# Optimization experiments

Hardware: AMD Instinct MI355X
Metric: run time of the kernel (lower is better)

The kernel has to match this reference:

```python
import jax, jax.numpy as jnp
import numpy as np

N_NODES = 50000
N_EDGES = 800000
D_FEAT = 64
N_GRAPHS = 512


def setup_inputs() -> dict:
    key = jax.random.key(0)
    ks = jax.random.split(key, 12)
    edge_index = jax.random.randint(ks[0], (2, N_EDGES), 0, N_NODES, dtype=jnp.int32)
    node_attr = jax.random.normal(ks[1], (N_NODES, D_FEAT), dtype=jnp.float32)
    edge_attr = jax.random.normal(ks[2], (N_EDGES, D_FEAT), dtype=jnp.float32)
    batch = jnp.sort(jax.random.randint(ks[3], (N_NODES,), 0, N_GRAPHS, dtype=jnp.int32))
    s = lambda fan_in: 1.0 / np.sqrt(fan_in)
    W_mpl = jax.random.uniform(ks[4], (3 * D_FEAT, 20), jnp.float32, -s(3 * D_FEAT), s(3 * D_FEAT))
    b_mpl = jnp.zeros((20,), jnp.float32)
    W1 = jax.random.uniform(ks[5], (20, 20), jnp.float32, -s(20), s(20))
    b1 = jnp.zeros((20,), jnp.float32)
    W2 = jax.random.uniform(ks[6], (20, 10), jnp.float32, -s(20), s(20))
    b2 = jnp.zeros((10,), jnp.float32)
    W3 = jax.random.uniform(ks[7], (10, 10), jnp.float32, -s(10), s(10))
    b3 = jnp.zeros((10,), jnp.float32)
    W4 = jax.random.uniform(ks[8], (10, 1), jnp.float32, -s(10), s(10))
    b4 = jnp.zeros((1,), jnp.float32)
    return {"edge_index": edge_index, "node_attr": node_attr, "edge_attr": edge_attr,
            "batch": batch, "W_mpl": W_mpl, "b_mpl": b_mpl, "W1": W1, "b1": b1,
            "W2": W2, "b2": b2, "W3": W3, "b3": b3, "W4": W4, "b4": b4}


def reference(edge_index, node_attr, edge_attr, batch,
              W_mpl, b_mpl, W1, b1, W2, b2, W3, b3, W4, b4):
    src, dst = edge_index[0], edge_index[1]
    # MPL_1: gather -> transform -> scatter-sum to destination nodes. [E, 3D] -> [E, 20]
    msg_in = jnp.concatenate([node_attr[src], node_attr[dst], edge_attr], axis=-1)
    msg = jax.nn.relu(msg_in @ W_mpl + b_mpl)
    x = jax.ops.segment_sum(msg, dst, num_segments=N_NODES)  # [N, 20]
    x = jax.nn.relu(x @ W1 + b1)
    x = jax.nn.relu(x @ W2 + b2)  # [N, 10]
    # segment_coo(reduce='sum') over graph ids -> [G, 10]
    x = jax.ops.segment_sum(x, batch, num_segments=N_GRAPHS)
    x = jax.nn.relu(x @ W3 + b3)
    return x @ W4 + b4  # [G, 1]
```

## Files before the change

kernel.cpp:

```cpp
#include <hip/hip_runtime.h>
#include <hip/hip_fp16.h>

#define DF 64
#define MSG 20
#define HID2 10
#define NODES 50000
#define EDGES 800000
#define GRAPHS 512
#define RSTRIDE 32
#define RS2 12
#define NB1 ((NODES + 255) / 256)
#define WR2 12

#define FMA20(acc, xv, wr) do { \
  float4 w0_ = *(const float4*)((wr) + 0);  float4 w1_ = *(const float4*)((wr) + 4); \
  float4 w2_ = *(const float4*)((wr) + 8);  float4 w3_ = *(const float4*)((wr) + 12); \
  float4 w4_ = *(const float4*)((wr) + 16); \
  acc[0]=fmaf(xv,w0_.x,acc[0]);  acc[1]=fmaf(xv,w0_.y,acc[1]);  acc[2]=fmaf(xv,w0_.z,acc[2]);  acc[3]=fmaf(xv,w0_.w,acc[3]); \
  acc[4]=fmaf(xv,w1_.x,acc[4]);  acc[5]=fmaf(xv,w1_.y,acc[5]);  acc[6]=fmaf(xv,w1_.z,acc[6]);  acc[7]=fmaf(xv,w1_.w,acc[7]); \
  acc[8]=fmaf(xv,w2_.x,acc[8]);  acc[9]=fmaf(xv,w2_.y,acc[9]);  acc[10]=fmaf(xv,w2_.z,acc[10]); acc[11]=fmaf(xv,w2_.w,acc[11]); \
  acc[12]=fmaf(xv,w3_.x,acc[12]); acc[13]=fmaf(xv,w3_.y,acc[13]); acc[14]=fmaf(xv,w3_.z,acc[14]); acc[15]=fmaf(xv,w3_.w,acc[15]); \
  acc[16]=fmaf(xv,w4_.x,acc[16]); acc[17]=fmaf(xv,w4_.y,acc[17]); acc[18]=fmaf(xv,w4_.z,acc[18]); acc[19]=fmaf(xv,w4_.w,acc[19]); \
} while (0)

__global__ __launch_bounds__(256) void zero_cnt_kernel(int* __restrict__ cnt) {
    int i = blockIdx.x * 256 + threadIdx.x;
    int st = gridDim.x * 256;
    for (int k = i; k < NODES; k += st) cnt[k] = 0;
}

__global__ __launch_bounds__(256) void count_kernel(const int* __restrict__ ei, int* __restrict__ cnt) {
    int e = blockIdx.x * 256 + threadIdx.x;
    if (e < EDGES) atomicAdd(&cnt[ei[EDGES + e]], 1);
}

__global__ __launch_bounds__(256) void scan_block(const int* __restrict__ in, int* __restrict__ outx,
                                                  int* __restrict__ bsum, int n) {
    __shared__ int s[256];
    int t = threadIdx.x, i = blockIdx.x * 256 + t;
    int v = (i < n) ? in[i] : 0;
    s[t] = v; __syncthreads();
    for (int off = 1; off < 256; off <<= 1) {
        int x = (t >= off) ? s[t - off] : 0;
        __syncthreads();
        s[t] += x; __syncthreads();
    }
    if (i < n) outx[i] = s[t] - v;
    if (t == 255 && bsum != nullptr) bsum[blockIdx.x] = s[255];
}

__device__ __forceinline__ void store_row_h(__half* dst, const float* acc) {
    union { __half2 h2[16]; uint4 q[4]; } u;
#pragma unroll
    for (int i = 0; i < 10; ++i) u.h2[i] = __floats2half2_rn(acc[2 * i], acc[2 * i + 1]);
#pragma unroll
    for (int i = 10; i < 16; ++i) u.h2[i] = __floats2half2_rn(0.0f, 0.0f);
    uint4* po = (uint4*)dst;
    po[0] = u.q[0]; po[1] = u.q[1]; po[2] = u.q[2]; po[3] = u.q[3];
}

__global__ __launch_bounds__(256) void fixup_pn_kernel(int* __restrict__ rs, int* __restrict__ cur,
                                                       const int* __restrict__ bscan,
                                                       const float* __restrict__ node_attr,
                                                       const float* __restrict__ W,
                                                       __half* __restrict__ Ps, __half* __restrict__ Pd) {
    int i = blockIdx.x * 256 + threadIdx.x;
    if (i < NODES) {
        int r = rs[i] + bscan[blockIdx.x];
        rs[i] = r;
        cur[i] = r;
    }
    if (i == 0) rs[NODES] = EDGES;

    __shared__ float Wss[DF * MSG];
    __shared__ float Wds[DF * MSG];
    for (int k = threadIdx.x; k < DF * MSG; k += 256) {
        Wss[k] = W[k];
        Wds[k] = W[DF * MSG + k];
    }
    __syncthreads();

    int n = i;
    if (n >= NODES) return;

    const float4* nr = (const float4*)(node_attr + (size_t)n * DF);
    float4 x[16];
#pragma unroll
    for (int q = 0; q < 16; ++q) x[q] = nr[q];

    float as[MSG], ad[MSG];
#pragma unroll
    for (int j = 0; j < MSG; ++j) { as[j] = 0.0f; ad[j] = 0.0f; }

#pragma unroll
    for (int k4 = 0; k4 < 16; ++k4) {
        const float* xp = (const float*)&x[k4];
#pragma unroll
        for (int cc = 0; cc < 4; ++cc) {
            int k = k4 * 4 + cc;
            FMA20(as, xp[cc], &Wss[k * MSG]);
            FMA20(ad, xp[cc], &Wds[k * MSG]);
        }
    }

    store_row_h(Ps + (size_t)n * RSTRIDE, as);
    store_row_h(Pd + (size_t)n * RSTRIDE, ad);
}

__global__ __launch_bounds__(256) void gbounds_kernel(const int* __restrict__ batch,
                                                      int* __restrict__ gstart) {
    int i = blockIdx.x * 256 + threadIdx.x;
    if (i < NODES) {
        int b = batch[i];
        int bp = (i == 0) ? -1 : batch[i - 1];
        for (int g = bp + 1; g <= b; ++g) gstart[g] = i;
        if (i == NODES - 1) {
            for (int g = b + 1; g <= GRAPHS; ++g) gstart[g] = NODES;
        }
    }
}

__device__ __forceinline__ __half2 shflx_h2(__half2 v, int mask) {
    int x; __builtin_memcpy(&x, &v, 4);
    x = __shfl_xor(x, mask, 4);
    __half2 r; __builtin_memcpy(&r, &x, 4);
    return r;
}

__device__ __forceinline__ __half2 sel4(int q, __half2 a, __half2 b, __half2 c, __half2 d) {
    __half2 ab = (q & 1) ? b : a;
    __half2 cd = (q & 1) ? d : c;
    return (q & 2) ? cd : ab;
}

__global__ __launch_bounds__(256, 4) void pe_quad_kernel(
    const int* __restrict__ ei,
    const float* __restrict__ edge_attr,
    const float* __restrict__ W, const float* __restrict__ b,
    const __half* __restrict__ Ps,
    int* __restrict__ cur,
    __half* __restrict__ PeP)
{
    __shared__ __half2 Wh2[64 * WR2];
    __shared__ __half2 bh[16];

    const int t = threadIdx.x;
    const int q = t & 3;
    const int e0 = blockIdx.x * 256 + (t >> 2) * 4;

    for (int i = t; i < 64 * WR2; i += 256) {
        int k = i / WR2, j = i - k * WR2;
        __half2 v = __floats2half2_rn(0.0f, 0.0f);
        if (j < 10) v = __floats2half2_rn(W[2 * DF * MSG + k * MSG + 2 * j],
                                          W[2 * DF * MSG + k * MSG + 2 * j + 1]);
        Wh2[i] = v;
    }
    if (t < 16) {
        __half2 v = __floats2half2_rn(0.0f, 0.0f);
        if (t < 10) v = __floats2half2_rn(b[2 * t], b[2 * t + 1]);
        bh[t] = v;
    }

    const int eq = e0 + q;
    const int srcq = ei[eq];
    const int dstq = ei[EDGES + eq];

    const float4* ea4 = (const float4*)edge_attr;
    __half2 xh[4][8];
#pragma unroll
    for (int i = 0; i < 4; ++i) {
        size_t rb = (size_t)(e0 + i) * 16 + q;
        float4 v0 = ea4[rb + 0];
        float4 v1 = ea4[rb + 4];
        float4 v2 = ea4[rb + 8];
        float4 v3 = ea4[rb + 12];
        xh[i][0] = __floats2half2_rn(v0.x, v0.y); xh[i][1] = __floats2half2_rn(v0.z, v0.w);
        xh[i][2] = __floats2half2_rn(v1.x, v1.y); xh[i][3] = __floats2half2_rn(v1.z, v1.w);
        xh[i][4] = __floats2half2_rn(v2.x, v2.y); xh[i][5] = __floats2half2_rn(v2.z, v2.w);
        xh[i][6] = __floats2half2_rn(v3.x, v3.y); xh[i][7] = __floats2half2_rn(v3.z, v3.w);
    }

    __syncthreads();

    __half2 acc[4][10];
#pragma unroll
    for (int i = 0; i < 4; ++i)
#pragma unroll
        for (int j = 0; j < 10; ++j) acc[i][j] = __floats2half2_rn(0.0f, 0.0f);

#pragma unroll
    for (int s = 0; s < 4; ++s) {
#pragma unroll
        for (int d = 0; d < 2; ++d) {
#pragma unroll
            for (int lh = 0; lh < 2; ++lh) {
                int k = s * 16 + q * 4 + 2 * d + lh;
                const __half2* wr = Wh2 + k * WR2;
                __half2 wa[10];
#pragma unroll
                for (int j = 0; j < 10; ++j) wa[j] = wr[j];
#pragma unroll
                for (int i = 0; i < 4; ++i) {
                    __half2 xb = lh ? __high2half2(xh[i][s * 2 + d])
                                    : __low2half2(xh[i][s * 2 + d]);
#pragma unroll
                    for (int j = 0; j < 10; ++j)
                        acc[i][j] = __hfma2(xb, wa[j], acc[i][j]);
                }
            }
        }
    }

#pragma unroll
    for (int i = 0; i < 4; ++i)
#pragma unroll
        for (int j = 0; j < 10; ++j) {
            acc[i][j] = __hadd2(acc[i][j], shflx_h2(acc[i][j], 1));
            acc[i][j] = __hadd2(acc[i][j], shflx_h2(acc[i][j], 2));
        }

#pragma unroll
    for (int i = 0; i < 4; ++i)
#pragma unroll
        for (int j = 0; j < 10; ++j) acc[i][j] = __hadd2(acc[i][j], bh[j]);

    int p = atomicAdd(&cur[dstq], 1);

    const __half2 hz = __floats2half2_rn(0.0f, 0.0f);
#pragma unroll
    for (int i = 0; i < 4; ++i) {
        int pi = __shfl(p, i, 4);
        int si = __shfl(srcq, i, 4);

        __half2 o0 = sel4(q, acc[i][0], acc[i][4], acc[i][8], hz);
        __half2 o1 = sel4(q, acc[i][1], acc[i][5], acc[i][9], hz);
        __half2 o2 = sel4(q, acc[i][2], acc[i][6], hz,        hz);
        __half2 o3 = sel4(q, acc[i][3], acc[i][7], hz,        hz);

        uint4 ps = *(const uint4*)(Ps + (size_t)si * RSTRIDE + q * 8);
        union { uint4 u; __half2 h[4]; } pu; pu.u = ps;
        union { uint4 u; __half2 h[4]; } ou;
        ou.h[0] = __hadd2(o0, pu.h[0]);
        ou.h[1] = __hadd2(o1, pu.h[1]);
        ou.h[2] = __hadd2(o2, pu.h[2]);
        ou.h[3] = __hadd2(o3, pu.h[3]);

        *(uint4*)(PeP + (size_t)pi * RSTRIDE + q * 8) = ou.u;
    }
}

__global__ __launch_bounds__(256, 4) void agg_kernel(const int* __restrict__ rs,
                                                     const __half* __restrict__ PeP,
                                                     const __half* __restrict__ Pd,
                                                     const float* __restrict__ W1, const float* __restrict__ b1,
                                                     const float* __restrict__ W2, const float* __restrict__ b2,
                                                     float* __restrict__ x2) {
    __shared__ float W1s[MSG * MSG], W2s[MSG * HID2], b1s[MSG], b2s[HID2];
    for (int i = threadIdx.x; i < MSG * MSG; i += 256) W1s[i] = W1[i];
    for (int i = threadIdx.x; i < MSG * HID2; i += 256) W2s[i] = W2[i];
    if (threadIdx.x < MSG) b1s[threadIdx.x] = b1[threadIdx.x];
    if (threadIdx.x < HID2) b2s[threadIdx.x] = b2[threadIdx.x];
    __syncthreads();

    int t = threadIdx.x;
    int node = blockIdx.x * 64 + (t >> 2);
    int lane = t & 3;

    float acc[MSG];
#pragma unroll
    for (int j = 0; j < MSG; ++j) acc[j] = 0.0f;

    if (node < NODES) {
        int s0 = rs[node];
        int deg = rs[node + 1] - s0;

        float pd[MSG];
        {
            const uint4* pr = (const uint4*)(Pd + (size_t)node * RSTRIDE);
            union { uint4 q; __half2 h2[4]; } a0, a1;
            union { uint2 q; __half2 h2[2]; } a2;
            a0.q = pr[0]; a1.q = pr[1]; a2.q = *(const uint2*)(pr + 2);
#pragma unroll
            for (int i = 0; i < 4; ++i) {
                float2 f = __half22float2(a0.h2[i]);
                pd[2 * i] = f.x; pd[2 * i + 1] = f.y;
            }
#pragma unroll
            for (int i = 0; i < 4; ++i) {
                float2 f = __half22float2(a1.h2[i]);
                pd[8 + 2 * i] = f.x; pd[9 + 2 * i] = f.y;
            }
#pragma unroll
            for (int i = 0; i < 2; ++i) {
                float2 f = __half22float2(a2.h2[i]);
                pd[16 + 2 * i] = f.x; pd[17 + 2 * i] = f.y;
            }
        }

        for (int i0 = lane; i0 < deg; i0 += 16) {
            uint4 qa[4], qb[4]; uint2 qc[4]; int vm[4];
#pragma unroll
            for (int u = 0; u < 4; ++u) {
                int i = i0 + 4 * u;
                vm[u] = (i < deg);
                if (vm[u]) {
                    const uint4* rp = (const uint4*)(PeP + (size_t)(s0 + i) * RSTRIDE);
                    qa[u] = rp[0]; qb[u] = rp[1]; qc[u] = *(const uint2*)(rp + 2);
                }
            }
#pragma unroll
            for (int u = 0; u < 4; ++u) {
                if (!vm[u]) continue;
                union { uint4 q; __half2 h2[4]; } a0, a1;
                union { uint2 q; __half2 h2[2]; } a2;
                a0.q = qa[u]; a1.q = qb[u]; a2.q = qc[u];
#pragma unroll
                for (int k = 0; k < 4; ++k) {
                    float2 f = __half22float2(a0.h2[k]);
                    acc[2 * k]     += fmaxf(f.x + pd[2 * k], 0.0f);
                    acc[2 * k + 1] += fmaxf(f.y + pd[2 * k + 1], 0.0f);
                }
#pragma unroll
                for (int k = 0; k < 4; ++k) {
                    float2 f = __half22float2(a1.h2[k]);
                    acc[8 + 2 * k] += fmaxf(f.x + pd[8 + 2 * k], 0.0f);
                    acc[9 + 2 * k] += fmaxf(f.y + pd[9 + 2 * k], 0.0f);
                }
#pragma unroll
                for (int k = 0; k < 2; ++k) {
                    float2 f = __half22float2(a2.h2[k]);
                    acc[16 + 2 * k] += fmaxf(f.x + pd[16 + 2 * k], 0.0f);
                    acc[17 + 2 * k] += fmaxf(f.y + pd[17 + 2 * k], 0.0f);
                }
            }
        }
    }

#pragma unroll
    for (int j = 0; j < MSG; ++j) acc[j] += __shfl_xor(acc[j], 1);
#pragma unroll
    for (int j = 0; j < MSG; ++j) acc[j] += __shfl_xor(acc[j], 2);

    if (node < NODES && lane == 0) {
        float t1[MSG];
#pragma unroll
        for (int j = 0; j < MSG; ++j) t1[j] = b1s[j];
#pragma unroll
        for (int k = 0; k < MSG; ++k)
#pragma unroll
            for (int j = 0; j < MSG; ++j) t1[j] = fmaf(acc[k], W1s[k * MSG + j], t1[j]);
#pragma unroll
        for (int j = 0; j < MSG; ++j) t1[j] = fmaxf(t1[j], 0.0f);

        float t2[HID2];
#pragma unroll
        for (int m = 0; m < HID2; ++m) t2[m] = b2s[m];
#pragma unroll
        for (int k = 0; k < MSG; ++k)
#pragma unroll
            for (int m = 0; m < HID2; ++m) t2[m] = fmaf(t1[k], W2s[k * HID2 + m], t2[m]);

        float* xo = x2 + (size_t)node * RS2;
        *(float4*)(xo)     = make_float4(fmaxf(t2[0], 0.f), fmaxf(t2[1], 0.f), fmaxf(t2[2], 0.f), fmaxf(t2[3], 0.f));
        *(float4*)(xo + 4) = make_float4(fmaxf(t2[4], 0.f), fmaxf(t2[5], 0.f), fmaxf(t2[6], 0.f), fmaxf(t2[7], 0.f));
        *(float4*)(xo + 8) = make_float4(fmaxf(t2[8], 0.f), fmaxf(t2[9], 0.f), 0.f, 0.f);
    }
}

__global__ __launch_bounds__(64) void graph2_kernel(const int* __restrict__ gstart,
                                                    const float* __restrict__ x2,
                                                    const float* __restrict__ W3, const float* __restrict__ b3,
                                                    const float* __restrict__ W4, const float* __restrict__ b4,
                                                    float* __restrict__ out) {
    int g = blockIdx.x;
    int lane = threadIdx.x;
    int n0 = gstart[g], n1 = gstart[g + 1];

    float acc[HID2];
#pragma unroll
    for (int j = 0; j < HID2; ++j) acc[j] = 0.0f;

    for (int i = n0 + lane; i < n1; i += 64) {
        const float* xr = x2 + (size_t)i * RS2;
        float4 v0 = *(const float4*)xr;
        float4 v1 = *(const float4*)(xr + 4);
        float2 v2 = *(const float2*)(xr + 8);
        acc[0] += v0.x; acc[1] += v0.y; acc[2] += v0.z; acc[3] += v0.w;
        acc[4] += v1.x; acc[5] += v1.y; acc[6] += v1.z; acc[7] += v1.w;
        acc[8] += v2.x; acc[9] += v2.y;
    }

#pragma unroll
    for (int m = 1; m < 64; m <<= 1)
#pragma unroll
        for (int j = 0; j < HID2; ++j) acc[j] += __shfl_xor(acc[j], m);

    if (lane == 0) {
        float tt[HID2];
#pragma unroll
        for (int j = 0; j < HID2; ++j) {
            float s = b3[j];
#pragma unroll
            for (int k = 0; k < HID2; ++k) s = fmaf(acc[k], W3[k * HID2 + j], s);
            tt[j] = fmaxf(s, 0.0f);
        }
        float s = b4[0];
#pragma unroll
        for (int k = 0; k < HID2; ++k) s = fmaf(tt[k], W4[k], s);
        out[g] = s;
    }
}

extern "C" void kernel_launch(void* const* d_in, const int* in_sizes, int n_in,
                              void* d_out, int out_size, void* d_ws, size_t ws_size,
                              hipStream_t stream) {
    const int*   ei        = (const int*)  d_in[0];
    const float* node_attr = (const float*)d_in[1];
    const float* edge_attr = (const float*)d_in[2];
    const int*   batch     = (const int*)  d_in[3];
    const float* W_mpl     = (const float*)d_in[4];
    const float* b_mpl     = (const float*)d_in[5];
    const float* W1        = (const float*)d_in[6];
    const float* b1        = (const float*)d_in[7];
    const float* W2        = (const float*)d_in[8];
    const float* b2        = (const float*)d_in[9];
    const float* W3        = (const float*)d_in[10];
    const float* b3        = (const float*)d_in[11];
    const float* W4        = (const float*)d_in[12];
    const float* b4        = (const float*)d_in[13];
    float* out = (float*)d_out;

    __half* PeP = (__half*)d_ws;
    __half* Ps  = PeP + (size_t)EDGES * RSTRIDE;
    __half* Pd  = Ps + (size_t)NODES * RSTRIDE;
    float* x2   = (float*)(Pd + (size_t)NODES * RSTRIDE);
    int* cnt    = (int*)(x2 + (size_t)NODES * RS2);
    int* rs     = cnt + 50176;
    int* cur    = rs + 50176;
    int* bsum   = cur + 50176;
    int* bscan  = bsum + 256;
    int* gstart = bscan + 256;

    int egrid  = (EDGES + 255) / 256;
    int ngrid  = NB1;

    hipLaunchKernelGGL(zero_cnt_kernel, dim3(256), dim3(256), 0, stream, cnt);
    hipLaunchKernelGGL(count_kernel, dim3(egrid), dim3(256), 0, stream, ei, cnt);
    hipLaunchKernelGGL(scan_block, dim3(ngrid), dim3(256), 0, stream, cnt, rs, bsum, NODES);
    hipLaunchKernelGGL(scan_block, dim3(1), dim3(256), 0, stream, bsum, bscan, (int*)nullptr, NB1);
    hipLaunchKernelGGL(fixup_pn_kernel, dim3(ngrid), dim3(256), 0, stream,
                       rs, cur, bscan, node_attr, W_mpl, Ps, Pd);
    hipLaunchKernelGGL(gbounds_kernel, dim3(ngrid), dim3(256), 0, stream, batch, gstart);
    hipLaunchKernelGGL(pe_quad_kernel, dim3(egrid), dim3(256), 0, stream,
                       ei, edge_attr, W_mpl, b_mpl, Ps, cur, PeP);
    hipLaunchKernelGGL(agg_kernel, dim3((NODES + 63) / 64), dim3(256), 0, stream,
                       rs, PeP, Pd, W1, b1, W2, b2, x2);
    hipLaunchKernelGGL(graph2_kernel, dim3(GRAPHS), dim3(64), 0, stream,
                       gstart, x2, W3, b3, W4, b4, out);
}
```

Before: 160.0 us.

## Record per-edge rank during counting to drop second atomic pass in edge kernel

The count kernel now stores the value returned by its atomic increment as a per-edge rank. The edge kernel then computes the CSR slot as row start plus rank instead of doing a second atomicAdd on a cursor array. This removes contended atomics from the edge-transform kernel at the cost of writing and reading an extra 800K-int rank array. The graph-bounds kernel is also folded into the fixup kernel to save one launch, and the aggregation loop now issues its loads unconditionally, clamping out-of-range indices, to avoid divergent branches.

```diff
diff --git a/kernel.cpp b/kernel.cpp
--- a/kernel.cpp
+++ b/kernel.cpp
@@ -29,9 +29,11 @@
     for (int k = i; k < NODES; k += st) cnt[k] = 0;
 }
 
-__global__ __launch_bounds__(256) void count_kernel(const int* __restrict__ ei, int* __restrict__ cnt) {
+__global__ __launch_bounds__(256) void count_kernel(const int* __restrict__ ei,
+                                                    int* __restrict__ cnt,
+                                                    int* __restrict__ rank) {
     int e = blockIdx.x * 256 + threadIdx.x;
-    if (e < EDGES) atomicAdd(&cnt[ei[EDGES + e]], 1);
+    if (e < EDGES) rank[e] = atomicAdd(&cnt[ei[EDGES + e]], 1);
 }
 
 __global__ __launch_bounds__(256) void scan_block(const int* __restrict__ in, int* __restrict__ outx,
@@ -59,16 +61,22 @@
     po[0] = u.q[0]; po[1] = u.q[1]; po[2] = u.q[2]; po[3] = u.q[3];
 }
 
-__global__ __launch_bounds__(256) void fixup_pn_kernel(int* __restrict__ rs, int* __restrict__ cur,
+__global__ __launch_bounds__(256) void fixup_pn_kernel(int* __restrict__ rs,
                                                        const int* __restrict__ bscan,
+                                                       const int* __restrict__ batch,
+                                                       int* __restrict__ gstart,
                                                        const float* __restrict__ node_attr,
                                                        const float* __restrict__ W,
                                                        __half* __restrict__ Ps, __half* __restrict__ Pd) {
     int i = blockIdx.x * 256 + threadIdx.x;
     if (i < NODES) {
-        int r = rs[i] + bscan[blockIdx.x];
-        rs[i] = r;
-        cur[i] = r;
+        rs[i] = rs[i] + bscan[blockIdx.x];
+        int b = batch[i];
+        int bp = (i == 0) ? -1 : batch[i - 1];
+        for (int g = bp + 1; g <= b; ++g) gstart[g] = i;
+        if (i == NODES - 1) {
+            for (int g = b + 1; g <= GRAPHS; ++g) gstart[g] = NODES;
+        }
     }
     if (i == 0) rs[NODES] = EDGES;
 
@@ -107,19 +115,6 @@
     store_row_h(Pd + (size_t)n * RSTRIDE, ad);
 }
 
-__global__ __launch_bounds__(256) void gbounds_kernel(const int* __restrict__ batch,
-                                                      int* __restrict__ gstart) {
-    int i = blockIdx.x * 256 + threadIdx.x;
-    if (i < NODES) {
-        int b = batch[i];
-        int bp = (i == 0) ? -1 : batch[i - 1];
-        for (int g = bp + 1; g <= b; ++g) gstart[g] = i;
-        if (i == NODES - 1) {
-            for (int g = b + 1; g <= GRAPHS; ++g) gstart[g] = NODES;
-        }
-    }
-}
-
 __device__ __forceinline__ __half2 shflx_h2(__half2 v, int mask) {
     int x; __builtin_memcpy(&x, &v, 4);
     x = __shfl_xor(x, mask, 4);
@@ -138,7 +133,8 @@
     const float* __restrict__ edge_attr,
     const float* __restrict__ W, const float* __restrict__ b,
     const __half* __restrict__ Ps,
-    int* __restrict__ cur,
+    const int* __restrict__ rs,
+    const int* __restrict__ rank,
     __half* __restrict__ PeP)
 {
     __shared__ __half2 Wh2[64 * WR2];
@@ -164,6 +160,7 @@
     const int eq = e0 + q;
     const int srcq = ei[eq];
     const int dstq = ei[EDGES + eq];
+    const int pq = rs[dstq] + rank[eq];
 
     const float4* ea4 = (const float4*)edge_attr;
     __half2 xh[4][8];
@@ -224,12 +221,10 @@
 #pragma unroll
         for (int j = 0; j < 10; ++j) acc[i][j] = __hadd2(acc[i][j], bh[j]);
 
-    int p = atomicAdd(&cur[dstq], 1);
-
     const __half2 hz = __floats2half2_rn(0.0f, 0.0f);
 #pragma unroll
     for (int i = 0; i < 4; ++i) {
-        int pi = __shfl(p, i, 4);
+        int pi = __shfl(pq, i, 4);
         int si = __shfl(srcq, i, 4);
 
         __half2 o0 = sel4(q, acc[i][0], acc[i][4], acc[i][8], hz);
@@ -303,10 +298,9 @@
             for (int u = 0; u < 4; ++u) {
                 int i = i0 + 4 * u;
                 vm[u] = (i < deg);
-                if (vm[u]) {
-                    const uint4* rp = (const uint4*)(PeP + (size_t)(s0 + i) * RSTRIDE);
-                    qa[u] = rp[0]; qb[u] = rp[1]; qc[u] = *(const uint2*)(rp + 2);
-                }
+                int ii = vm[u] ? i : 0;
+                const uint4* rp = (const uint4*)(PeP + (size_t)(s0 + ii) * RSTRIDE);
+                qa[u] = rp[0]; qb[u] = rp[1]; qc[u] = *(const uint2*)(rp + 2);
             }
 #pragma unroll
             for (int u = 0; u < 4; ++u) {
@@ -436,8 +430,8 @@
     float* x2   = (float*)(Pd + (size_t)NODES * RSTRIDE);
     int* cnt    = (int*)(x2 + (size_t)NODES * RS2);
     int* rs     = cnt + 50176;
-    int* cur    = rs + 50176;
-    int* bsum   = cur + 50176;
+    int* rank   = rs + 50176;
+    int* bsum   = rank + EDGES;
     int* bscan  = bsum + 256;
     int* gstart = bscan + 256;
 
@@ -445,14 +439,13 @@
     int ngrid  = NB1;
 
     hipLaunchKernelGGL(zero_cnt_kernel, dim3(256), dim3(256), 0, stream, cnt);
-    hipLaunchKernelGGL(count_kernel, dim3(egrid), dim3(256), 0, stream, ei, cnt);
+    hipLaunchKernelGGL(count_kernel, dim3(egrid), dim3(256), 0, stream, ei, cnt, rank);
     hipLaunchKernelGGL(scan_block, dim3(ngrid), dim3(256), 0, stream, cnt, rs, bsum, NODES);
     hipLaunchKernelGGL(scan_block, dim3(1), dim3(256), 0, stream, bsum, bscan, (int*)nullptr, NB1);
     hipLaunchKernelGGL(fixup_pn_kernel, dim3(ngrid), dim3(256), 0, stream,
-                       rs, cur, bscan, node_attr, W_mpl, Ps, Pd);
-    hipLaunchKernelGGL(gbounds_kernel, dim3(ngrid), dim3(256), 0, stream, batch, gstart);
+                       rs, bscan, batch, gstart, node_attr, W_mpl, Ps, Pd);
     hipLaunchKernelGGL(pe_quad_kernel, dim3(egrid), dim3(256), 0, stream,
-                       ei, edge_attr, W_mpl, b_mpl, Ps, cur, PeP);
+                       ei, edge_attr, W_mpl, b_mpl, Ps, rs, rank, PeP);
     hipLaunchKernelGGL(agg_kernel, dim3((NODES + 63) / 64), dim3(256), 0, stream,
                        rs, PeP, Pd, W1, b1, W2, b2, x2);
     hipLaunchKernelGGL(graph2_kernel, dim3(GRAPHS), dim3(64), 0, stream,
```

Measured after the change: 146.0 us. 1.1x faster.
